# Kernel tuning notes

Hardware: AMD Instinct MI355X
Metric: run time of the kernel (lower is better)

Reference implementation:

```python
import jax, jax.numpy as jnp
import numpy as np

HEADS = 8
DIM_HEAD = 64
EPS = 1e-5


def _layernorm(x, g, b):
    m = jnp.mean(x, axis=-1, keepdims=True)
    v = jnp.mean((x - m) ** 2, axis=-1, keepdims=True)
    return (x - m) * jax.lax.rsqrt(v + EPS) * g + b


def setup_inputs() -> dict:
    key = jax.random.key(0)
    ks = jax.random.split(key, 8)
    b, c, hh, ww = 4, 256, 48, 48
    inner = HEADS * DIM_HEAD  # 512
    s = 0.02
    return {
        "x": jax.random.normal(ks[0], (b, c, hh, ww), jnp.float32),
        "Wq": jax.random.normal(ks[1], (c, inner), jnp.float32) * s,
        "Wk": jax.random.normal(ks[2], (c, inner), jnp.float32) * s,
        "Wv": jax.random.normal(ks[3], (c, inner), jnp.float32) * s,
        "Wo": jax.random.normal(ks[4], (inner, c), jnp.float32) * s,
        "bo": jnp.zeros((c,), jnp.float32),
        "g1": jnp.ones((c,), jnp.float32),
        "b1": jnp.zeros((c,), jnp.float32),
        "g2": jnp.ones((c,), jnp.float32),
        "b2": jnp.zeros((c,), jnp.float32),
        "Wf1": jax.random.normal(ks[5], (c, 2 * c), jnp.float32) * s,
        "bf1": jnp.zeros((2 * c,), jnp.float32),
        "Wf2": jax.random.normal(ks[6], (2 * c, c), jnp.float32) * s,
        "bf2": jnp.zeros((c,), jnp.float32),
        "Wp": jax.random.normal(ks[7], (c, c), jnp.float32) * s,
        "bp": jnp.zeros((c,), jnp.float32),
    }


def reference(x, Wq, Wk, Wv, Wo, bo, g1, b1, g2, b2, Wf1, bf1, Wf2, bf2, Wp, bp):
    b, c, hh, ww = x.shape
    n = hh * ww
    scale = DIM_HEAD ** -0.5
    x_in = x
    t = jnp.transpose(x.reshape(b, c, n), (0, 2, 1))  # [b, n, c]

    # --- CrossAttention (self-attn, context=None) ---
    tn = _layernorm(t, g1, b1)
    q = (tn @ Wq).reshape(b, n, HEADS, DIM_HEAD)
    k = (tn @ Wk).reshape(b, n, HEADS, DIM_HEAD)
    v = (tn @ Wv).reshape(b, n, HEADS, DIM_HEAD)
    sim = jnp.einsum("bihd,bjhd->bhij", q, k) * scale  # [b,h,n,n]
    attn = jax.nn.softmax(sim, axis=-1)
    o = jnp.einsum("bhij,bjhd->bihd", attn, v).reshape(b, n, HEADS * DIM_HEAD)
    t = o @ Wo + bo + t

    # --- FeedForward: Linear -> GELU(exact) -> Linear ---
    f = jax.nn.gelu(_layernorm(t, g2, b2) @ Wf1 + bf1, approximate=False)
    t = f @ Wf2 + bf2 + t

    # back to image and 1x1 conv (Wp[c_in, c_out])
    xi = jnp.transpose(t, (0, 2, 1)).reshape(b, c, hh, ww)
    y = jnp.einsum("bchw,co->bohw", xi, Wp) + bp[None, :, None, None]
    return y + x_in
```

## Files before the change

kernel.cpp:

```cpp
#include <hip/hip_runtime.h>
#include <math.h>

#define B_    4
#define C_    256
#define N_    2304
#define H_    8
#define DH_   64
#define IN_   512
#define ROWS_ 9216
#define NHALF 576

typedef __attribute__((ext_vector_type(8))) short short8;
typedef __attribute__((ext_vector_type(4))) float f32x4;
typedef __attribute__((ext_vector_type(16))) float f32x16;

__device__ __forceinline__ unsigned short f2bf(float f) {
    unsigned int u = __float_as_uint(f);
    u += 0x7fffu + ((u >> 16) & 1u);
    return (unsigned short)(u >> 16);
}

__device__ __forceinline__ float bf2f(unsigned short u) {
    return __uint_as_float(((unsigned)u) << 16);
}

__device__ __forceinline__ float gelu_exact(float x) {
    return 0.5f * x * (1.0f + erff(x * 0.70710678118654752440f));
}

__device__ __forceinline__ unsigned cvtpk(float lo, float hi) {
    unsigned r;
    asm("v_cvt_pk_bf16_f32 %0, %1, %2" : "=v"(r) : "v"(lo), "v"(hi));
    return r;
}

__device__ __forceinline__ void gload_lds16(const void* g, void* l) {
    __builtin_amdgcn_global_load_lds(
        (const __attribute__((address_space(1))) unsigned int*)g,
        (__attribute__((address_space(3))) unsigned int*)l, 16, 0, 0);
}

__device__ __forceinline__ const short8* frg(const short* base, int row, int chunk) {
    return (const short8*)(base + (row << 6) + (((chunk) ^ (row & 7)) << 3));
}

__device__ __forceinline__ int swz2(int row) {
    return (row & 7) ^ ((row >> 3) & 3);
}
__device__ __forceinline__ const short8* frg2(const short* base, int row, int chunk) {
    return (const short8*)(base + (row << 6) + (((chunk) ^ swz2(row)) << 3));
}

__global__ __launch_bounds__(256)
void k_trans_ln(const float* __restrict__ x, float* __restrict__ T,
                unsigned short* __restrict__ TNh,
                const float* __restrict__ g, const float* __restrict__ b) {
    __shared__ float tile[32][257];
    int bb = blockIdx.y;
    int nBase = blockIdx.x * 32;
    int tid = threadIdx.x;
    int tx = tid & 31;
    int tg = tid >> 5;
    const float* xp = x + (size_t)bb * C_ * N_ + nBase + tx;
    #pragma unroll
    for (int i = 0; i < 32; ++i) {
        int c = tg * 32 + i;
        tile[tx][c] = xp[(size_t)c * N_];
    }
    __syncthreads();
    int w = tid >> 6, lane = tid & 63;
    float g0 = g[lane], g1 = g[lane + 64], g2 = g[lane + 128], g3 = g[lane + 192];
    float b0 = b[lane], b1 = b[lane + 64], b2 = b[lane + 128], b3 = b[lane + 192];
    #pragma unroll
    for (int r8 = 0; r8 < 8; ++r8) {
        int row = w * 8 + r8;
        float v0 = tile[row][lane],       v1 = tile[row][lane + 64];
        float v2 = tile[row][lane + 128], v3 = tile[row][lane + 192];
        float s = v0 + v1 + v2 + v3;
        #pragma unroll
        for (int m = 1; m < 64; m <<= 1) s += __shfl_xor(s, m);
        float mean = s * (1.0f / C_);
        float d0 = v0 - mean, d1 = v1 - mean, d2 = v2 - mean, d3 = v3 - mean;
        float s2 = d0 * d0 + d1 * d1 + d2 * d2 + d3 * d3;
        #pragma unroll
        for (int m = 1; m < 64; m <<= 1) s2 += __shfl_xor(s2, m);
        float rs = rsqrtf(s2 * (1.0f / C_) + 1e-5f);
        size_t o = (size_t)(bb * N_ + nBase + row) * C_ + lane;
        T[o]       = v0; T[o + 64]  = v1; T[o + 128] = v2; T[o + 192] = v3;
        TNh[o]       = f2bf(d0 * rs * g0 + b0);
        TNh[o + 64]  = f2bf(d1 * rs * g1 + b1);
        TNh[o + 128] = f2bf(d2 * rs * g2 + b2);
        TNh[o + 192] = f2bf(d3 * rs * g3 + b3);
    }
}

__global__ __launch_bounds__(256)
void k_prep(const float* __restrict__ Wq, const float* __restrict__ Wk,
            const float* __restrict__ Wv, const float* __restrict__ Wo,
            const float* __restrict__ Wf1, const float* __restrict__ Wf2,
            const float* __restrict__ Wp,
            unsigned short* Wqh, unsigned short* Wkh, unsigned short* Wvh,
            unsigned short* Woh, unsigned short* Wf1h, unsigned short* Wf2h,
            unsigned short* Wph) {
    const float* src; unsigned short* dst; int K, N;
    switch (blockIdx.z) {
        case 0: src = Wq;  dst = Wqh;  K = 256; N = 512; break;
        case 1: src = Wk;  dst = Wkh;  K = 256; N = 512; break;
        case 2: src = Wv;  dst = Wvh;  K = 256; N = 512; break;
        case 3: src = Wo;  dst = Woh;  K = 512; N = 256; break;
        case 4: src = Wf1; dst = Wf1h; K = 256; N = 512; break;
        case 5: src = Wf2; dst = Wf2h; K = 512; N = 256; break;
        default: src = Wp; dst = Wph;  K = 256; N = 256; break;
    }
    float scl = (blockIdx.z == 0) ? 0.18033688f : 1.0f;
    int nBase = blockIdx.x * 32;
    int kBase = blockIdx.y * 32;
    if (nBase >= N || kBase >= K) return;
    __shared__ float tile[32][33];
    int tx = threadIdx.x, ty = threadIdx.y;
    #pragma unroll
    for (int i = 0; i < 32; i += 8)
        tile[ty + i][tx] = src[(size_t)(kBase + ty + i) * N + nBase + tx];
    __syncthreads();
    #pragma unroll
    for (int i = 0; i < 32; i += 8)
        dst[(size_t)(nBase + ty + i) * K + kBase + tx] = f2bf(tile[tx][ty + i] * scl);
}

__global__ __launch_bounds__(256)
void k_layernorm_bf16(const float* __restrict__ in, unsigned short* __restrict__ out,
                      const float* __restrict__ g, const float* __restrict__ b) {
    int wv = threadIdx.x >> 6;
    int lane = threadIdx.x & 63;
    int row = blockIdx.x * 4 + wv;
    float4 v = ((const float4*)(in + (size_t)row * C_))[lane];
    float s = v.x + v.y + v.z + v.w;
    #pragma unroll
    for (int m = 1; m < 64; m <<= 1) s += __shfl_xor(s, m);
    float mean = s * (1.0f / C_);
    float dx = v.x - mean, dy = v.y - mean, dz = v.z - mean, dw = v.w - mean;
    float s2 = dx * dx + dy * dy + dz * dz + dw * dw;
    #pragma unroll
    for (int m = 1; m < 64; m <<= 1) s2 += __shfl_xor(s2, m);
    float rs = rsqrtf(s2 * (1.0f / C_) + 1e-5f);
    float4 gv = ((const float4*)g)[lane];
    float4 bv = ((const float4*)b)[lane];
    ushort4 o;
    o.x = f2bf(dx * rs * gv.x + bv.x);
    o.y = f2bf(dy * rs * gv.y + bv.y);
    o.z = f2bf(dz * rs * gv.z + bv.z);
    o.w = f2bf(dw * rs * gv.w + bv.w);
    *(ushort4*)(out + (size_t)row * C_ + lane * 4) = o;
}

template <int EP>
__global__ __launch_bounds__(256)
void k_gemm64(const short* __restrict__ A, const short* __restrict__ Bt,
              void* __restrict__ Out, const float* __restrict__ bias,
              const float* __restrict__ Res, int M, int N, int K) {
    __shared__ __align__(16) short As[64 * 64];
    __shared__ __align__(16) short Bs[64 * 64];
    int tid = threadIdx.x;
    int w = tid >> 6;
    int lane = tid & 63;
    int l15 = lane & 15;
    int lg = lane >> 4;
    int wr = w >> 1, wc = w & 1;
    int rowBase = blockIdx.y * 64;
    int colBase = blockIdx.x * 64;

    f32x4 acc[2][2];
    #pragma unroll
    for (int m = 0; m < 2; ++m)
        #pragma unroll
        for (int n = 0; n < 2; ++n) acc[m][n] = (f32x4){0.f, 0.f, 0.f, 0.f};

    for (int k0 = 0; k0 < K; k0 += 64) {
        __syncthreads();
        #pragma unroll
        for (int a = 0; a < 2; ++a) {
            int rr = (w << 4) + (a << 3) + (lane >> 3);
            int cc = (lane & 7) ^ (lane >> 3);
            gload_lds16(A + (size_t)(rowBase + rr) * K + k0 + cc * 8,
                        As + (((w << 4) + (a << 3)) << 6));
            gload_lds16(Bt + (size_t)(colBase + rr) * K + k0 + cc * 8,
                        Bs + (((w << 4) + (a << 3)) << 6));
        }
        asm volatile("s_waitcnt vmcnt(0)" ::: "memory");
        __syncthreads();
        short8 af[2][2], bf[2][2];
        #pragma unroll
        for (int m = 0; m < 2; ++m) {
            af[m][0] = *frg(As, wr * 32 + m * 16 + l15, lg);
            af[m][1] = *frg(As, wr * 32 + m * 16 + l15, 4 + lg);
        }
        #pragma unroll
        for (int n = 0; n < 2; ++n) {
            bf[n][0] = *frg(Bs, wc * 32 + n * 16 + l15, lg);
            bf[n][1] = *frg(Bs, wc * 32 + n * 16 + l15, 4 + lg);
        }
        #pragma unroll
        for (int m = 0; m < 2; ++m)
            #pragma unroll
            for (int n = 0; n < 2; ++n) {
                acc[m][n] = __builtin_amdgcn_mfma_f32_16x16x32_bf16(af[m][0], bf[n][0], acc[m][n], 0, 0, 0);
                acc[m][n] = __builtin_amdgcn_mfma_f32_16x16x32_bf16(af[m][1], bf[n][1], acc[m][n], 0, 0, 0);
            }
    }

    int arB = rowBase + wr * 32;
    int brB = colBase + wc * 32;
    int bb = 0;
    if (EP == 5) bb = brB / N_;
    #pragma unroll
    for (int m = 0; m < 2; ++m) {
        #pragma unroll
        for (int i = 0; i < 4; ++i) {
            int ar = arB + m * 16 + lg * 4 + i;
            #pragma unroll
            for (int n = 0; n < 2; ++n) {
                int br = brB + n * 16 + l15;
                float v = acc[m][n][i];
                if constexpr (EP == 2) {
                    size_t o = (size_t)ar * N + br;
                    ((float*)Out)[o] = v + bias[br] + Res[o];
                } else if constexpr (EP == 3) {
                    ((unsigned short*)Out)[(size_t)ar * N + br] = f2bf(gelu_exact(v + bias[br]));
                } else if constexpr (EP == 4) {
                    size_t o = (size_t)ar * N + br;
                    ((unsigned short*)Out)[o] = f2bf(v + bias[br] + Res[o]);
                } else {
                    size_t o = ((size_t)(bb * C_) + ar) * N_ + (br - bb * N_);
                    ((float*)Out)[o] = v + bias[ar] + Res[o];
                }
            }
        }
    }
}

__global__ __launch_bounds__(256)
void k_gemm_qkv(const short* __restrict__ TNh, const short* __restrict__ Wqh,
                const short* __restrict__ Wkh, const short* __restrict__ Wvh,
                unsigned short* __restrict__ Qb, unsigned short* __restrict__ Kb,
                unsigned short* __restrict__ Vt) {
    __shared__ __align__(16) short As[128 * 64];
    __shared__ __align__(16) short Bs[128 * 64];
    int tid = threadIdx.x;
    int w = tid >> 6;
    int lane = tid & 63;
    int l15 = lane & 15;
    int lg = lane >> 4;
    int wr = w >> 1, wc = w & 1;
    int z = blockIdx.y;
    const short *A, *Bt;
    int rowBase, colBase;
    if (z < 2) {
        A = TNh; Bt = z ? Wkh : Wqh;
        colBase = (blockIdx.x & 3) * 128;
        rowBase = (blockIdx.x >> 2) * 128;
    } else {
        A = Wvh; Bt = TNh;
        colBase = (blockIdx.x % 72) * 128;
        rowBase = (blockIdx.x / 72) * 128;
    }
    const int K = C_;

    f32x4 acc[4][4];
    #pragma unroll
    for (int m = 0; m < 4; ++m)
        #pragma unroll
        for (int n = 0; n < 4; ++n) acc[m][n] = (f32x4){0.f, 0.f, 0.f, 0.f};

    for (int k0 = 0; k0 < K; k0 += 64) {
        __syncthreads();
        #pragma unroll
        for (int a = 0; a < 4; ++a) {
            int rr = (w << 5) + (a << 3) + (lane >> 3);
            int cc = (lane & 7) ^ (lane >> 3);
            gload_lds16(A + (size_t)(rowBase + rr) * K + k0 + cc * 8,
                        As + (((w << 5) + (a << 3)) << 6));
            gload_lds16(Bt + (size_t)(colBase + rr) * K + k0 + cc * 8,
                        Bs + (((w << 5) + (a << 3)) << 6));
        }
        asm volatile("s_waitcnt vmcnt(0)" ::: "memory");
        __syncthreads();
        short8 af[4][2], bf[4][2];
        #pragma unroll
        for (int m = 0; m < 4; ++m) {
            af[m][0] = *frg(As, wr * 64 + m * 16 + l15, lg);
            af[m][1] = *frg(As, wr * 64 + m * 16 + l15, 4 + lg);
        }
        #pragma unroll
        for (int n = 0; n < 4; ++n) {
            bf[n][0] = *frg(Bs, wc * 64 + n * 16 + l15, lg);
            bf[n][1] = *frg(Bs, wc * 64 + n * 16 + l15, 4 + lg);
        }
        #pragma unroll
        for (int m = 0; m < 4; ++m)
            #pragma unroll
            for (int n = 0; n < 4; ++n) {
                acc[m][n] = __builtin_amdgcn_mfma_f32_16x16x32_bf16(af[m][0], bf[n][0], acc[m][n], 0, 0, 0);
                acc[m][n] = __builtin_amdgcn_mfma_f32_16x16x32_bf16(af[m][1], bf[n][1], acc[m][n], 0, 0, 0);
            }
    }

    int arB = rowBase + wr * 64;
    int brB = colBase + wc * 64;
    if (z < 2) {
        unsigned short* Out = z ? Kb : Qb;
        #pragma unroll
        for (int m = 0; m < 4; ++m)
            #pragma unroll
            for (int i = 0; i < 4; ++i) {
                int ar = arB + m * 16 + lg * 4 + i;
                #pragma unroll
                for (int n = 0; n < 4; ++n)
                    Out[(size_t)ar * IN_ + brB + n * 16 + l15] = f2bf(acc[m][n][i]);
            }
    } else {
        int bb = brB / N_;
        #pragma unroll
        for (int m = 0; m < 4; ++m)
            #pragma unroll
            for (int i = 0; i < 4; ++i) {
                int ar = arB + m * 16 + lg * 4 + i;
                #pragma unroll
                for (int n = 0; n < 4; ++n) {
                    int br = brB + n * 16 + l15;
                    Vt[((size_t)(bb * IN_) + ar) * N_ + (br - bb * N_)] = f2bf(acc[m][n][i]);
                }
            }
    }
}

__global__ __launch_bounds__(256)
void k_flash_mfma(const short* __restrict__ Qb, const short* __restrict__ Kb,
                  const short* __restrict__ Vt,
                  unsigned short* O0, unsigned short* O1,
                  unsigned short* O2, unsigned short* O3,
                  float* __restrict__ Lsum) {
    __shared__ __align__(16) short Ks[64 * 64];
    __shared__ __align__(16) short Vs[64 * 64];
    int tid = threadIdx.x;
    int lane = tid & 63;
    int l31 = lane & 31;
    int h5 = lane >> 5;
    int w = tid >> 6;

    int logical = (blockIdx.x & 7) * 288 + (blockIdx.x >> 3);
    int pair = logical / 18;
    int qi = logical - pair * 18;
    int bh = pair & 31;
    int half = pair >> 5;
    int bb = bh >> 3, h = bh & 7;
    int qBase = qi * 128;
    int h0 = half * NHALF;

    const short* Qp = Qb + ((size_t)bb * N_ + qBase + w * 32) * IN_ + h * DH_;
    const short* Kp = Kb + (size_t)bb * N_ * IN_ + h * DH_;
    const short* Vp = Vt + ((size_t)bb * IN_ + h * DH_) * N_;

    short8 qf[4];
    #pragma unroll
    for (int kk = 0; kk < 4; ++kk)
        qf[kk] = *(const short8*)(Qp + (size_t)l31 * IN_ + kk * 16 + h5 * 8);

    short8 ones;
    #pragma unroll
    for (int j = 0; j < 8; ++j) ones[j] = (short)0x3F80;

    int r0s = tid >> 3, c0s = tid & 7;
    int r1s = (tid + 256) >> 3, c1s = tid & 7;
    int w0s = (c0s ^ swz2(r0s)) << 3;
    int w1s = (c1s ^ swz2(r1s)) << 3;
    uint4 kreg0 = *(const uint4*)(Kp + (size_t)(h0 + r0s) * IN_ + c0s * 8);
    uint4 kreg1 = *(const uint4*)(Kp + (size_t)(h0 + r1s) * IN_ + c1s * 8);
    uint4 vreg0 = *(const uint4*)(Vp + (size_t)r0s * N_ + h0 + c0s * 8);
    uint4 vreg1 = *(const uint4*)(Vp + (size_t)r1s * N_ + h0 + c1s * 8);

    f32x16 oacc0 = (f32x16)(0.0f);
    f32x16 oacc1 = (f32x16)(0.0f);
    f32x16 lacc  = (f32x16)(0.0f);

    for (int kt = h0; kt < h0 + NHALF; kt += 64) {
        __syncthreads();
        *(uint4*)(Ks + (r0s << 6) + w0s) = kreg0;
        *(uint4*)(Ks + (r1s << 6) + w1s) = kreg1;
        *(uint4*)(Vs + (r0s << 6) + w0s) = vreg0;
        *(uint4*)(Vs + (r1s << 6) + w1s) = vreg1;
        if (kt + 64 < h0 + NHALF) {
            kreg0 = *(const uint4*)(Kp + (size_t)(kt + 64 + r0s) * IN_ + c0s * 8);
            kreg1 = *(const uint4*)(Kp + (size_t)(kt + 64 + r1s) * IN_ + c1s * 8);
            vreg0 = *(const uint4*)(Vp + (size_t)r0s * N_ + kt + 64 + c0s * 8);
            vreg1 = *(const uint4*)(Vp + (size_t)r1s * N_ + kt + 64 + c1s * 8);
        }
        __syncthreads();

        short8 pa[4];
        #pragma unroll
        for (int s = 0; s < 2; ++s) {
            f32x16 stv = (f32x16)(0.0f);
            #pragma unroll
            for (int kk = 0; kk < 4; ++kk) {
                short8 kf = *frg2(Ks, s * 32 + l31, kk * 2 + h5);
                stv = __builtin_amdgcn_mfma_f32_32x32x16_bf16(kf, qf[kk], stv, 0, 0, 0);
            }
            unsigned u[8];
            #pragma unroll
            for (int q = 0; q < 4; ++q) {
                u[2 * q]     = cvtpk(exp2f(stv[4 * q + 0]), exp2f(stv[4 * q + 1]));
                u[2 * q + 1] = cvtpk(exp2f(stv[4 * q + 2]), exp2f(stv[4 * q + 3]));
            }
            asm volatile("v_permlane32_swap_b32 %0, %1" : "+v"(u[0]), "+v"(u[2]));
            asm volatile("v_permlane32_swap_b32 %0, %1" : "+v"(u[1]), "+v"(u[3]));
            asm volatile("v_permlane32_swap_b32 %0, %1" : "+v"(u[4]), "+v"(u[6]));
            asm volatile("v_permlane32_swap_b32 %0, %1" : "+v"(u[5]), "+v"(u[7]));
            union { unsigned uu[4]; short8 s8; } c0, c1;
            c0.uu[0] = u[0]; c0.uu[1] = u[1]; c0.uu[2] = u[2]; c0.uu[3] = u[3];
            c1.uu[0] = u[4]; c1.uu[1] = u[5]; c1.uu[2] = u[6]; c1.uu[3] = u[7];
            pa[2 * s]     = c0.s8;
            pa[2 * s + 1] = c1.s8;
        }

        #pragma unroll
        for (int kk = 0; kk < 4; ++kk) {
            short8 vf0 = *frg2(Vs, l31, kk * 2 + h5);
            short8 vf1 = *frg2(Vs, 32 + l31, kk * 2 + h5);
            lacc  = __builtin_amdgcn_mfma_f32_32x32x16_bf16(pa[kk], ones, lacc, 0, 0, 0);
            oacc0 = __builtin_amdgcn_mfma_f32_32x32x16_bf16(pa[kk], vf0, oacc0, 0, 0, 0);
            oacc1 = __builtin_amdgcn_mfma_f32_32x32x16_bf16(pa[kk], vf1, oacc1, 0, 0, 0);
        }
    }

    unsigned short* OpH = (half == 0) ? O0 : (half == 1) ? O1 : (half == 2) ? O2 : O3;
    unsigned short* Op = OpH + ((size_t)bb * N_ + qBase + w * 32) * IN_ + h * DH_;
    #pragma unroll
    for (int reg = 0; reg < 16; ++reg) {
        int q = (reg & 3) + 8 * (reg >> 2) + 4 * h5;
        Op[(size_t)q * IN_ + l31]      = f2bf(oacc0[reg]);
        Op[(size_t)q * IN_ + 32 + l31] = f2bf(oacc1[reg]);
    }
    if (l31 == 0) {
        float* Lp = Lsum + (((size_t)half * B_ + bb) * H_ + h) * N_ + qBase + w * 32;
        #pragma unroll
        for (int reg = 0; reg < 16; ++reg) {
            int q = (reg & 3) + 8 * (reg >> 2) + 4 * h5;
            Lp[q] = lacc[reg];
        }
    }
}

__global__ __launch_bounds__(256)
void k_combine(const unsigned short* p0, const unsigned short* p1,
               const unsigned short* p2, const unsigned short* p3,
               const float* __restrict__ Lsum, unsigned short* Ob) {
    int wv = threadIdx.x >> 6;
    int lane = threadIdx.x & 63;
    int row = blockIdx.x * 4 + wv;
    int bb = row / N_;
    int n = row - bb * N_;
    int hh = lane >> 3;
    float l = 0.f;
    #pragma unroll
    for (int q4 = 0; q4 < 4; ++q4)
        l += Lsum[(((size_t)q4 * B_ + bb) * H_ + hh) * N_ + n];
    float inv = 1.0f / l;
    size_t off = (size_t)row * IN_ + lane * 8;
    short8 a0 = *(const short8*)(p0 + off);
    short8 a1 = *(const short8*)(p1 + off);
    short8 a2 = *(const short8*)(p2 + off);
    short8 a3 = *(const short8*)(p3 + off);
    unsigned short o[8];
    #pragma unroll
    for (int j = 0; j < 8; ++j)
        o[j] = f2bf((bf2f((unsigned short)a0[j]) + bf2f((unsigned short)a1[j]) +
                     bf2f((unsigned short)a2[j]) + bf2f((unsigned short)a3[j])) * inv);
    *(uint4*)(Ob + off) = *(uint4*)o;
}

extern "C" void kernel_launch(void* const* d_in, const int* in_sizes, int n_in,
                              void* d_out, int out_size, void* d_ws, size_t ws_size,
                              hipStream_t stream) {
    (void)in_sizes; (void)n_in; (void)out_size; (void)ws_size;
    const float* x   = (const float*)d_in[0];
    const float* Wq  = (const float*)d_in[1];
    const float* Wk  = (const float*)d_in[2];
    const float* Wv  = (const float*)d_in[3];
    const float* Wo  = (const float*)d_in[4];
    const float* bo  = (const float*)d_in[5];
    const float* g1  = (const float*)d_in[6];
    const float* b1  = (const float*)d_in[7];
    const float* g2  = (const float*)d_in[8];
    const float* b2  = (const float*)d_in[9];
    const float* Wf1 = (const float*)d_in[10];
    const float* bf1 = (const float*)d_in[11];
    const float* Wf2 = (const float*)d_in[12];
    const float* bf2 = (const float*)d_in[13];
    const float* Wp  = (const float*)d_in[14];
    const float* bp  = (const float*)d_in[15];
    float* out = (float*)d_out;
    float* ws  = (float*)d_ws;

    float* T    = ws;
    float* T2   = ws + 2359296;
    unsigned short* TNh = (unsigned short*)(ws + 4718592);
    short* Qb   = (short*)(ws + 5898240);
    short* Kb   = (short*)(ws + 8257536);
    short* Vt   = (short*)(ws + 10616832);
    unsigned short* Obh = (unsigned short*)(ws + 12976128);
    short* F    = (short*)(ws + 15335424);
    short* T3h  = (short*)(ws + 17694720);
    unsigned short* Wqh  = (unsigned short*)(ws + 18874368);
    unsigned short* Wkh  = (unsigned short*)(ws + 18939904);
    unsigned short* Wvh  = (unsigned short*)(ws + 19005440);
    unsigned short* Woh  = (unsigned short*)(ws + 19070976);
    unsigned short* Wf1h = (unsigned short*)(ws + 19136512);
    unsigned short* Wf2h = (unsigned short*)(ws + 19202048);
    unsigned short* Wph  = (unsigned short*)(ws + 19267584);
    unsigned short* Op0  = (unsigned short*)(ws + 19398656);
    unsigned short* Op3  = (unsigned short*)(ws + 21757952);
    unsigned short* Op1  = Obh;
    unsigned short* Op2  = (unsigned short*)F;
    float* Lsum = ws + 24117248;

    k_prep<<<dim3(16, 16, 7), dim3(32, 8), 0, stream>>>(Wq, Wk, Wv, Wo, Wf1, Wf2, Wp,
                                                        Wqh, Wkh, Wvh, Woh, Wf1h, Wf2h, Wph);
    k_trans_ln<<<dim3(72, 4), 256, 0, stream>>>(x, T, TNh, g1, b1);
    k_gemm_qkv<<<dim3(288, 3), 256, 0, stream>>>((const short*)TNh, (const short*)Wqh,
                                                 (const short*)Wkh, (const short*)Wvh,
                                                 (unsigned short*)Qb, (unsigned short*)Kb,
                                                 (unsigned short*)Vt);
    k_flash_mfma<<<dim3(2304), 256, 0, stream>>>(Qb, Kb, Vt, Op0, Op1, Op2, Op3, Lsum);
    k_combine<<<2304, 256, 0, stream>>>(Op0, Op1, Op2, Op3, Lsum, Obh);
    k_gemm64<2><<<dim3(4, 144), 256, 0, stream>>>((const short*)Obh, (const short*)Woh, T2, bo, T, ROWS_, C_, IN_);
    k_layernorm_bf16<<<2304, 256, 0, stream>>>(T2, TNh, g2, b2);
    k_gemm64<3><<<dim3(8, 144), 256, 0, stream>>>((const short*)TNh, (const short*)Wf1h, F, bf1, nullptr, ROWS_, IN_, C_);
    k_gemm64<4><<<dim3(4, 144), 256, 0, stream>>>((const short*)F, (const short*)Wf2h, T3h, bf2, T2, ROWS_, C_, IN_);
    k_gemm64<5><<<dim3(144, 4), 256, 0, stream>>>((const short*)Wph, (const short*)T3h, out, bp, x, C_, ROWS_, C_);
}
```

Before: 162.0 us.

## Merge weight prep with transpose-LN, shrink QKV GEMM tiles, add MFMA priority hints

Combines the weight-conversion kernel and the transpose+layernorm kernel into one launch that picks its role from the block index, which drops one kernel launch. The QKV GEMM moves from 128x128 to 64x64 tiles with a flat 1D grid, giving four times as many blocks to fill the CUs. The flash attention kernel wraps its MFMA sections in s_setprio calls so waves issuing matrix work get higher scheduling priority. Smaller tiles reduce operand reuse per block, and the merged kernel runs both roles at the same 256-thread shape.

Measured after the change: 155.7 us. -3.9%, faster.

```diff
diff --git a/kernel.cpp b/kernel.cpp
--- a/kernel.cpp
+++ b/kernel.cpp
@@ -52,79 +52,82 @@
 }
 
 __global__ __launch_bounds__(256)
-void k_trans_ln(const float* __restrict__ x, float* __restrict__ T,
-                unsigned short* __restrict__ TNh,
-                const float* __restrict__ g, const float* __restrict__ b) {
+void k_pre(const float* __restrict__ Wq, const float* __restrict__ Wk,
+           const float* __restrict__ Wv, const float* __restrict__ Wo,
+           const float* __restrict__ Wf1, const float* __restrict__ Wf2,
+           const float* __restrict__ Wp,
+           unsigned short* Wqh, unsigned short* Wkh, unsigned short* Wvh,
+           unsigned short* Woh, unsigned short* Wf1h, unsigned short* Wf2h,
+           unsigned short* Wph,
+           const float* __restrict__ x, float* __restrict__ T,
+           unsigned short* __restrict__ TNh,
+           const float* __restrict__ g1, const float* __restrict__ b1) {
     __shared__ float tile[32][257];
-    int bb = blockIdx.y;
-    int nBase = blockIdx.x * 32;
+    int bid = blockIdx.x;
     int tid = threadIdx.x;
-    int tx = tid & 31;
-    int tg = tid >> 5;
-    const float* xp = x + (size_t)bb * C_ * N_ + nBase + tx;
-    #pragma unroll
-    for (int i = 0; i < 32; ++i) {
-        int c = tg * 32 + i;
-        tile[tx][c] = xp[(size_t)c * N_];
-    }
-    __syncthreads();
-    int w = tid >> 6, lane = tid & 63;
-    float g0 = g[lane], g1 = g[lane + 64], g2 = g[lane + 128], g3 = g[lane + 192];
-    float b0 = b[lane], b1 = b[lane + 64], b2 = b[lane + 128], b3 = b[lane + 192];
-    #pragma unroll
-    for (int r8 = 0; r8 < 8; ++r8) {
-        int row = w * 8 + r8;
-        float v0 = tile[row][lane],       v1 = tile[row][lane + 64];
-        float v2 = tile[row][lane + 128], v3 = tile[row][lane + 192];
-        float s = v0 + v1 + v2 + v3;
-        #pragma unroll
-        for (int m = 1; m < 64; m <<= 1) s += __shfl_xor(s, m);
-        float mean = s * (1.0f / C_);
-        float d0 = v0 - mean, d1 = v1 - mean, d2 = v2 - mean, d3 = v3 - mean;
-        float s2 = d0 * d0 + d1 * d1 + d2 * d2 + d3 * d3;
-        #pragma unroll
-        for (int m = 1; m < 64; m <<= 1) s2 += __shfl_xor(s2, m);
-        float rs = rsqrtf(s2 * (1.0f / C_) + 1e-5f);
-        size_t o = (size_t)(bb * N_ + nBase + row) * C_ + lane;
-        T[o]       = v0; T[o + 64]  = v1; T[o + 128] = v2; T[o + 192] = v3;
-        TNh[o]       = f2bf(d0 * rs * g0 + b0);
-        TNh[o + 64]  = f2bf(d1 * rs * g1 + b1);
-        TNh[o + 128] = f2bf(d2 * rs * g2 + b2);
-        TNh[o + 192] = f2bf(d3 * rs * g3 + b3);
-    }
-}
-
-__global__ __launch_bounds__(256)
-void k_prep(const float* __restrict__ Wq, const float* __restrict__ Wk,
-            const float* __restrict__ Wv, const float* __restrict__ Wo,
-            const float* __restrict__ Wf1, const float* __restrict__ Wf2,
-            const float* __restrict__ Wp,
-            unsigned short* Wqh, unsigned short* Wkh, unsigned short* Wvh,
-            unsigned short* Woh, unsigned short* Wf1h, unsigned short* Wf2h,
-            unsigned short* Wph) {
-    const float* src; unsigned short* dst; int K, N;
-    switch (blockIdx.z) {
-        case 0: src = Wq;  dst = Wqh;  K = 256; N = 512; break;
-        case 1: src = Wk;  dst = Wkh;  K = 256; N = 512; break;
-        case 2: src = Wv;  dst = Wvh;  K = 256; N = 512; break;
-        case 3: src = Wo;  dst = Woh;  K = 512; N = 256; break;
-        case 4: src = Wf1; dst = Wf1h; K = 256; N = 512; break;
-        case 5: src = Wf2; dst = Wf2h; K = 512; N = 256; break;
-        default: src = Wp; dst = Wph;  K = 256; N = 256; break;
-    }
-    float scl = (blockIdx.z == 0) ? 0.18033688f : 1.0f;
-    int nBase = blockIdx.x * 32;
-    int kBase = blockIdx.y * 32;
-    if (nBase >= N || kBase >= K) return;
-    __shared__ float tile[32][33];
-    int tx = threadIdx.x, ty = threadIdx.y;
-    #pragma unroll
-    for (int i = 0; i < 32; i += 8)
-        tile[ty + i][tx] = src[(size_t)(kBase + ty + i) * N + nBase + tx];
-    __syncthreads();
-    #pragma unroll
-    for (int i = 0; i < 32; i += 8)
-        dst[(size_t)(nBase + ty + i) * K + kBase + tx] = f2bf(tile[tx][ty + i] * scl);
+    if (bid < 1792) {
+        int wz = bid >> 8;
+        int rem = bid & 255;
+        int nBase = (rem & 15) * 32;
+        int kBase = (rem >> 4) * 32;
+        const float* src; unsigned short* dst; int K, N;
+        switch (wz) {
+            case 0: src = Wq;  dst = Wqh;  K = 256; N = 512; break;
+            case 1: src = Wk;  dst = Wkh;  K = 256; N = 512; break;
+            case 2: src = Wv;  dst = Wvh;  K = 256; N = 512; break;
+            case 3: src = Wo;  dst = Woh;  K = 512; N = 256; break;
+            case 4: src = Wf1; dst = Wf1h; K = 256; N = 512; break;
+            case 5: src = Wf2; dst = Wf2h; K = 512; N = 256; break;
+            default: src = Wp; dst = Wph;  K = 256; N = 256; break;
+        }
+        if (nBase >= N || kBase >= K) return;
+        float scl = (wz == 0) ? 0.18033688f : 1.0f;
+        int tx = tid & 31, ty = tid >> 5;
+        #pragma unroll
+        for (int i = 0; i < 32; i += 8)
+            tile[ty + i][tx] = src[(size_t)(kBase + ty + i) * N + nBase + tx];
+        __syncthreads();
+        #pragma unroll
+        for (int i = 0; i < 32; i += 8)
+            dst[(size_t)(nBase + ty + i) * K + kBase + tx] = f2bf(tile[tx][ty + i] * scl);
+    } else {
+        int idx = bid - 1792;
+        int bb = idx / 72;
+        int nBase = (idx - bb * 72) * 32;
+        int tx = tid & 31;
+        int tg = tid >> 5;
+        const float* xp = x + (size_t)bb * C_ * N_ + nBase + tx;
+        #pragma unroll
+        for (int i = 0; i < 32; ++i) {
+            int c = tg * 32 + i;
+            tile[tx][c] = xp[(size_t)c * N_];
+        }
+        __syncthreads();
+        int w = tid >> 6, lane = tid & 63;
+        float g0 = g1[lane], ga = g1[lane + 64], gb2 = g1[lane + 128], gc = g1[lane + 192];
+        float b0 = b1[lane], ba = b1[lane + 64], bb2 = b1[lane + 128], bc = b1[lane + 192];
+        #pragma unroll
+        for (int r8 = 0; r8 < 8; ++r8) {
+            int row = w * 8 + r8;
+            float v0 = tile[row][lane],       v1 = tile[row][lane + 64];
+            float v2 = tile[row][lane + 128], v3 = tile[row][lane + 192];
+            float s = v0 + v1 + v2 + v3;
+            #pragma unroll
+            for (int m = 1; m < 64; m <<= 1) s += __shfl_xor(s, m);
+            float mean = s * (1.0f / C_);
+            float d0 = v0 - mean, d1 = v1 - mean, d2 = v2 - mean, d3 = v3 - mean;
+            float s2 = d0 * d0 + d1 * d1 + d2 * d2 + d3 * d3;
+            #pragma unroll
+            for (int m = 1; m < 64; m <<= 1) s2 += __shfl_xor(s2, m);
+            float rs = rsqrtf(s2 * (1.0f / C_) + 1e-5f);
+            size_t o = (size_t)(bb * N_ + nBase + row) * C_ + lane;
+            T[o]       = v0; T[o + 64]  = v1; T[o + 128] = v2; T[o + 192] = v3;
+            TNh[o]       = f2bf(d0 * rs * g0 + b0);
+            TNh[o + 64]  = f2bf(d1 * rs * ga + ba);
+            TNh[o + 128] = f2bf(d2 * rs * gb2 + bb2);
+            TNh[o + 192] = f2bf(d3 * rs * gc + bc);
+        }
+    }
 }
 
 __global__ __launch_bounds__(256)
@@ -243,89 +246,91 @@
                 const short* __restrict__ Wkh, const short* __restrict__ Wvh,
                 unsigned short* __restrict__ Qb, unsigned short* __restrict__ Kb,
                 unsigned short* __restrict__ Vt) {
-    __shared__ __align__(16) short As[128 * 64];
-    __shared__ __align__(16) short Bs[128 * 64];
+    __shared__ __align__(16) short As[64 * 64];
+    __shared__ __align__(16) short Bs[64 * 64];
+    int bid = blockIdx.x;
+    int z = bid / 1152;
+    int rem = bid - z * 1152;
     int tid = threadIdx.x;
     int w = tid >> 6;
     int lane = tid & 63;
     int l15 = lane & 15;
     int lg = lane >> 4;
     int wr = w >> 1, wc = w & 1;
-    int z = blockIdx.y;
     const short *A, *Bt;
     int rowBase, colBase;
     if (z < 2) {
         A = TNh; Bt = z ? Wkh : Wqh;
-        colBase = (blockIdx.x & 3) * 128;
-        rowBase = (blockIdx.x >> 2) * 128;
+        colBase = (rem & 7) * 64;
+        rowBase = (rem >> 3) * 64;
     } else {
         A = Wvh; Bt = TNh;
-        colBase = (blockIdx.x % 72) * 128;
-        rowBase = (blockIdx.x / 72) * 128;
+        colBase = (rem % 144) * 64;
+        rowBase = (rem / 144) * 64;
     }
     const int K = C_;
 
-    f32x4 acc[4][4];
-    #pragma unroll
-    for (int m = 0; m < 4; ++m)
-        #pragma unroll
-        for (int n = 0; n < 4; ++n) acc[m][n] = (f32x4){0.f, 0.f, 0.f, 0.f};
+    f32x4 acc[2][2];
+    #pragma unroll
+    for (int m = 0; m < 2; ++m)
+        #pragma unroll
+        for (int n = 0; n < 2; ++n) acc[m][n] = (f32x4){0.f, 0.f, 0.f, 0.f};
 
     for (int k0 = 0; k0 < K; k0 += 64) {
         __syncthreads();
         #pragma unroll
-        for (int a = 0; a < 4; ++a) {
-            int rr = (w << 5) + (a << 3) + (lane >> 3);
+        for (int a = 0; a < 2; ++a) {
+            int rr = (w << 4) + (a << 3) + (lane >> 3);
             int cc = (lane & 7) ^ (lane >> 3);
             gload_lds16(A + (size_t)(rowBase + rr) * K + k0 + cc * 8,
-                        As + (((w << 5) + (a << 3)) << 6));
+                        As + (((w << 4) + (a << 3)) << 6));
             gload_lds16(Bt + (size_t)(colBase + rr) * K + k0 + cc * 8,
-                        Bs + (((w << 5) + (a << 3)) << 6));
+                        Bs + (((w << 4) + (a << 3)) << 6));
         }
         asm volatile("s_waitcnt vmcnt(0)" ::: "memory");
         __syncthreads();
-        short8 af[4][2], bf[4][2];
-        #pragma unroll
-        for (int m = 0; m < 4; ++m) {
-            af[m][0] = *frg(As, wr * 64 + m * 16 + l15, lg);
-            af[m][1] = *frg(As, wr * 64 + m * 16 + l15, 4 + lg);
-        }
-        #pragma unroll
-        for (int n = 0; n < 4; ++n) {
-            bf[n][0] = *frg(Bs, wc * 64 + n * 16 + l15, lg);
-            bf[n][1] = *frg(Bs, wc * 64 + n * 16 + l15, 4 + lg);
-        }
-        #pragma unroll
-        for (int m = 0; m < 4; ++m)
-            #pragma unroll
-            for (int n = 0; n < 4; ++n) {
+        short8 af[2][2], bf[2][2];
+        #pragma unroll
+        for (int m = 0; m < 2; ++m) {
+            af[m][0] = *frg(As, wr * 32 + m * 16 + l15, lg);
+            af[m][1] = *frg(As, wr * 32 + m * 16 + l15, 4 + lg);
+        }
+        #pragma unroll
+        for (int n = 0; n < 2; ++n) {
+            bf[n][0] = *frg(Bs, wc * 32 + n * 16 + l15, lg);
+            bf[n][1] = *frg(Bs, wc * 32 + n * 16 + l15, 4 + lg);
+        }
+        #pragma unroll
+        for (int m = 0; m < 2; ++m)
+            #pragma unroll
+            for (int n = 0; n < 2; ++n) {
                 acc[m][n] = __builtin_amdgcn_mfma_f32_16x16x32_bf16(af[m][0], bf[n][0], acc[m][n], 0, 0, 0);
                 acc[m][n] = __builtin_amdgcn_mfma_f32_16x16x32_bf16(af[m][1], bf[n][1], acc[m][n], 0, 0, 0);
             }
     }
 
-    int arB = rowBase + wr * 64;
-    int brB = colBase + wc * 64;
+    int arB = rowBase + wr * 32;
+    int brB = colBase + wc * 32;
     if (z < 2) {
         unsigned short* Out = z ? Kb : Qb;
         #pragma unroll
-        for (int m = 0; m < 4; ++m)
+        for (int m = 0; m < 2; ++m)
             #pragma unroll
             for (int i = 0; i < 4; ++i) {
                 int ar = arB + m * 16 + lg * 4 + i;
                 #pragma unroll
-                for (int n = 0; n < 4; ++n)
+                for (int n = 0; n < 2; ++n)
                     Out[(size_t)ar * IN_ + brB + n * 16 + l15] = f2bf(acc[m][n][i]);
             }
     } else {
         int bb = brB / N_;
         #pragma unroll
-        for (int m = 0; m < 4; ++m)
+        for (int m = 0; m < 2; ++m)
             #pragma unroll
             for (int i = 0; i < 4; ++i) {
                 int ar = arB + m * 16 + lg * 4 + i;
                 #pragma unroll
-                for (int n = 0; n < 4; ++n) {
+                for (int n = 0; n < 2; ++n) {
                     int br = brB + n * 16 + l15;
                     Vt[((size_t)(bb * IN_) + ar) * N_ + (br - bb * N_)] = f2bf(acc[m][n][i]);
                 }
@@ -400,11 +405,13 @@
         #pragma unroll
         for (int s = 0; s < 2; ++s) {
             f32x16 stv = (f32x16)(0.0f);
+            __builtin_amdgcn_s_setprio(1);
             #pragma unroll
             for (int kk = 0; kk < 4; ++kk) {
                 short8 kf = *frg2(Ks, s * 32 + l31, kk * 2 + h5);
                 stv = __builtin_amdgcn_mfma_f32_32x32x16_bf16(kf, qf[kk], stv, 0, 0, 0);
             }
+            __builtin_amdgcn_s_setprio(0);
             unsigned u[8];
             #pragma unroll
             for (int q = 0; q < 4; ++q) {
@@ -422,6 +429,7 @@
             pa[2 * s + 1] = c1.s8;
         }
 
+        __builtin_amdgcn_s_setprio(1);
         #pragma unroll
         for (int kk = 0; kk < 4; ++kk) {
             short8 vf0 = *frg2(Vs, l31, kk * 2 + h5);
@@ -430,6 +438,7 @@
             oacc0 = __builtin_amdgcn_mfma_f32_32x32x16_bf16(pa[kk], vf0, oacc0, 0, 0, 0);
             oacc1 = __builtin_amdgcn_mfma_f32_32x32x16_bf16(pa[kk], vf1, oacc1, 0, 0, 0);
         }
+        __builtin_amdgcn_s_setprio(0);
     }
 
     unsigned short* OpH = (half == 0) ? O0 : (half == 1) ? O1 : (half == 2) ? O2 : O3;
@@ -523,13 +532,13 @@
     unsigned short* Op2  = (unsigned short*)F;
     float* Lsum = ws + 24117248;
 
-    k_prep<<<dim3(16, 16, 7), dim3(32, 8), 0, stream>>>(Wq, Wk, Wv, Wo, Wf1, Wf2, Wp,
-                                                        Wqh, Wkh, Wvh, Woh, Wf1h, Wf2h, Wph);
-    k_trans_ln<<<dim3(72, 4), 256, 0, stream>>>(x, T, TNh, g1, b1);
-    k_gemm_qkv<<<dim3(288, 3), 256, 0, stream>>>((const short*)TNh, (const short*)Wqh,
-                                                 (const short*)Wkh, (const short*)Wvh,
-                                                 (unsigned short*)Qb, (unsigned short*)Kb,
-                                                 (unsigned short*)Vt);
+    k_pre<<<dim3(2080), 256, 0, stream>>>(Wq, Wk, Wv, Wo, Wf1, Wf2, Wp,
+                                          Wqh, Wkh, Wvh, Woh, Wf1h, Wf2h, Wph,
+                                          x, T, TNh, g1, b1);
+    k_gemm_qkv<<<dim3(3456), 256, 0, stream>>>((const short*)TNh, (const short*)Wqh,
+                                               (const short*)Wkh, (const short*)Wvh,
+                                               (unsigned short*)Qb, (unsigned short*)Kb,
+                                               (unsigned short*)Vt);
     k_flash_mfma<<<dim3(2304), 256, 0, stream>>>(Qb, Kb, Vt, Op0, Op1, Op2, Op3, Lsum);
     k_combine<<<2304, 256, 0, stream>>>(Op0, Op1, Op2, Op3, Lsum, Obh);
     k_gemm64<2><<<dim3(4, 144), 256, 0, stream>>>((const short*)Obh, (const short*)Woh, T2, bo, T, ROWS_, C_, IN_);
```
